# Performance work log

Measured on AMD Instinct MI355X. Metric: run time of the kernel, lower is better.

Reference implementation:

```python
import jax, jax.numpy as jnp
import numpy as np

N = 100000   # nodes
E = 400000   # edges
G = 5000     # graphs (20 nodes each)
H = 128      # hidden_channels
ATOM_D, BOND_D, BOOL_D = 16, 8, 2
NODE_D = 30 + ATOM_D + 3 * BOOL_D   # 52
EDGE_D = 2 + BOND_D + 3 * BOOL_D    # 16


def setup_inputs() -> dict:
    key = jax.random.key(0)
    ks = jax.random.split(key, 24)
    rn = lambda k, shape: jax.random.normal(k, shape, dtype=jnp.float32) * 0.05
    # node features: [atom_idx, 10 continuous, 3 bools]
    atom_idx = jax.random.randint(ks[0], (N,), 1, 119)
    node_cont = jax.random.normal(ks[1], (N, 10), dtype=jnp.float32)
    node_bool = jax.random.randint(ks[2], (N, 3), 0, 2)
    x = jnp.concatenate([atom_idx[:, None].astype(jnp.float32), node_cont,
                         node_bool.astype(jnp.float32)], axis=1)
    # edge features: [bond_idx, 1 continuous, 3 bools]
    bond_idx = jax.random.randint(ks[3], (E,), 1, 22)
    edge_cont = jax.random.normal(ks[4], (E, 1), dtype=jnp.float32)
    edge_bool = jax.random.randint(ks[5], (E, 3), 0, 2)
    edge_attr = jnp.concatenate([bond_idx[:, None].astype(jnp.float32), edge_cont,
                                 edge_bool.astype(jnp.float32)], axis=1)
    edge_index = jax.random.randint(ks[6], (2, E), 0, N)
    batch = jnp.repeat(jnp.arange(G, dtype=jnp.int32), N // G)
    # embeddings (with padding rows zeroed, as nn.Embedding padding_idx)
    atom_emb = rn(ks[7], (119, ATOM_D)).at[0].set(0.0)
    bond_emb = rn(ks[8], (22, BOND_D)).at[0].set(0.0)
    bool_emb = rn(ks[9], (3, BOOL_D)).at[2].set(0.0)
    Wn = rn(ks[10], (10, 30)); bn = jnp.zeros((30,), jnp.float32)
    We = rn(ks[11], (1, 2));   be = jnp.zeros((2,), jnp.float32)
    Wl1 = rn(ks[12], (NODE_D, H)); bl1 = jnp.zeros((H,), jnp.float32)
    Wr1 = rn(ks[13], (NODE_D, H)); br1 = jnp.zeros((H,), jnp.float32)
    Wedge1 = rn(ks[14], (EDGE_D, H)); att1 = rn(ks[15], (H,))
    bias1 = jnp.zeros((H,), jnp.float32)
    Wl2 = rn(ks[16], (H, H)); bl2 = jnp.zeros((H,), jnp.float32)
    Wr2 = rn(ks[17], (H, H)); br2 = jnp.zeros((H,), jnp.float32)
    Wedge2 = rn(ks[18], (EDGE_D, H)); att2 = rn(ks[19], (H,))
    bias2 = jnp.zeros((H,), jnp.float32)
    return dict(x=x, edge_index=edge_index, edge_attr=edge_attr, batch=batch,
                atom_emb=atom_emb, bond_emb=bond_emb, bool_emb=bool_emb,
                Wn=Wn, bn=bn, We=We, be=be,
                Wl1=Wl1, bl1=bl1, Wr1=Wr1, br1=br1, Wedge1=Wedge1, att1=att1, bias1=bias1,
                Wl2=Wl2, bl2=bl2, Wr2=Wr2, br2=br2, Wedge2=Wedge2, att2=att2, bias2=bias2)


def _gatv2(h, src, dst, e_lin, Wl, bl, Wr, br, att, bias):
    # PyG GATv2Conv, heads=1: xl = lin_l(x) (source), xr = lin_r(x) (target)
    xl = h @ Wl + bl
    xr = h @ Wr + br
    m = xl[src] + xr[dst] + e_lin                      # [E', H]
    a = jax.nn.leaky_relu(m, 0.2) @ att                # [E']
    amax = jax.ops.segment_max(a, dst, num_segments=N)
    ex = jnp.exp(a - amax[dst])
    denom = jax.ops.segment_sum(ex, dst, num_segments=N)
    alpha = ex / denom[dst]                            # softmax over incoming edges
    out = jax.ops.segment_sum(alpha[:, None] * xl[src], dst, num_segments=N)
    return out + bias


def reference(x, edge_index, edge_attr, batch,
              atom_emb, bond_emb, bool_emb, Wn, bn, We, be,
              Wl1, bl1, Wr1, br1, Wedge1, att1, bias1,
              Wl2, bl2, Wr2, br2, Wedge2, att2, bias2):
    # --- encode nodes ---
    ai = x[:, 0].astype(jnp.int32)
    nb = x[:, 11:14].astype(jnp.int32)
    h = jnp.concatenate([atom_emb[ai], x[:, 1:11] @ Wn + bn,
                         bool_emb[nb[:, 0]], bool_emb[nb[:, 1]], bool_emb[nb[:, 2]]], axis=1)
    # --- encode edges ---
    bi = edge_attr[:, 0].astype(jnp.int32)
    eb = edge_attr[:, 2:5].astype(jnp.int32)
    e = jnp.concatenate([bond_emb[bi], edge_attr[:, 1:2] @ We + be,
                         bool_emb[eb[:, 0]], bool_emb[eb[:, 1]], bool_emb[eb[:, 2]]], axis=1)
    src, dst = edge_index[0], edge_index[1]
    # --- add self loops with fill_value='mean' (mean of in-edge attrs per node) ---
    cnt = jax.ops.segment_sum(jnp.ones((E,), h.dtype), dst, num_segments=N)
    loop_attr = jax.ops.segment_sum(e, dst, num_segments=N) / jnp.maximum(cnt, 1.0)[:, None]
    e_full = jnp.concatenate([e, loop_attr], axis=0)          # [E+N, EDGE_D]
    loop = jnp.arange(N, dtype=src.dtype)
    src_f = jnp.concatenate([src, loop])
    dst_f = jnp.concatenate([dst, loop])
    # --- 3 GATv2 layers (layers 2 and 3 share weights, as in the original) ---
    h = jax.nn.relu(_gatv2(h, src_f, dst_f, e_full @ Wedge1, Wl1, bl1, Wr1, br1, att1, bias1))
    e_lin2 = e_full @ Wedge2
    h = jax.nn.relu(_gatv2(h, src_f, dst_f, e_lin2, Wl2, bl2, Wr2, br2, att2, bias2))
    h = jax.nn.relu(_gatv2(h, src_f, dst_f, e_lin2, Wl2, bl2, Wr2, br2, att2, bias2))
    # --- global_max_pool readout ---
    return jax.ops.segment_max(h, batch, num_segments=G)
```

## Files before the change

### kernel.cpp

```cpp
#include <hip/hip_runtime.h>
#include <hip/hip_fp16.h>

#define N_NODES 100000
#define N_EDGES 400000
#define N_GRAPHS 5000
#define NPG 20
#define SCAN_NB 256
#define SCAN_CHUNK ((N_NODES + SCAN_NB - 1) / SCAN_NB)
#define TAB_STRIDE (256 * 128 + 128)
#define F1 8192
#define F2 16384
#define NB_ENC ((N_NODES + 255) / 256)
#define NB_HIST ((N_EDGES + 255) / 256)

typedef __attribute__((ext_vector_type(8))) _Float16 f16x8;
typedef __attribute__((ext_vector_type(2))) _Float16 h2;
typedef __attribute__((ext_vector_type(4))) float f32x4;

#define DPP_QUAD_XOR1 0xB1
#define DPP_QUAD_XOR2 0x4E
#define DPP_ROW_HALF_MIRROR 0x141
#define DPP_ROW_MIRROR 0x140
template <int CTRL>
__device__ __forceinline__ float dpp_add(float x) {
  int p = __builtin_amdgcn_update_dpp(0, __float_as_int(x), CTRL, 0xf, 0xf, true);
  return x + __int_as_float(p);
}

__global__ __launch_bounds__(256) void k_prologue(
    const float* __restrict__ x, const float* __restrict__ atom_emb,
    const float* __restrict__ bool_emb, const float* __restrict__ Wn,
    const float* __restrict__ bn, __half* __restrict__ h0,
    const int* __restrict__ dst, int* __restrict__ cnt,
    const float* __restrict__ Wedge1, const float* __restrict__ Wedge2,
    const float* __restrict__ bond_emb, const float* __restrict__ We,
    const float* __restrict__ be, __half* __restrict__ tabs,
    const float* __restrict__ Wl1, const float* __restrict__ Wr1,
    const float* __restrict__ Wl2, const float* __restrict__ Wr2,
    unsigned short* __restrict__ fr) {
  int b = blockIdx.x, tid = threadIdx.x;
  if (b < NB_ENC) {
    int n = b * 256 + tid;
    if (n >= N_NODES) return;
    const float* xr = x + (size_t)n * 14;
    int ai = (int)xr[0];
    _Float16 hr[64];
    #pragma unroll
    for (int j = 0; j < 16; j++) hr[j] = (_Float16)atom_emb[ai * 16 + j];
    float xc[10];
    #pragma unroll
    for (int k = 0; k < 10; k++) xc[k] = xr[1 + k];
    #pragma unroll
    for (int c = 0; c < 30; c++) {
      float s = bn[c];
      #pragma unroll
      for (int k = 0; k < 10; k++) s += xc[k] * Wn[k * 30 + c];
      hr[16 + c] = (_Float16)s;
    }
    #pragma unroll
    for (int t = 0; t < 3; t++) {
      int bb = (int)xr[11 + t];
      hr[46 + 2 * t]     = (_Float16)bool_emb[2 * bb];
      hr[46 + 2 * t + 1] = (_Float16)bool_emb[2 * bb + 1];
    }
    #pragma unroll
    for (int j = 52; j < 64; j++) hr[j] = (_Float16)0.0f;
    uint4* d4 = (uint4*)(h0 + (size_t)n * 64);
    const uint4* s4 = (const uint4*)hr;
    #pragma unroll
    for (int j = 0; j < 8; j++) d4[j] = s4[j];
  } else if (b < NB_ENC + NB_HIST) {
    int e = (b - NB_ENC) * 256 + tid;
    if (e >= N_EDGES) return;
    atomicAdd(cnt + dst[e], 1);
  } else if (b == NB_ENC + NB_HIST) {
    int s = tid >> 7, c = tid & 127;
    const float* W = s ? Wedge2 : Wedge1;
    __half* T12 = tabs + (size_t)s * TAB_STRIDE;
    __half* v   = T12 + 256 * 128;
    float w8 = W[8 * 128 + c], w9 = W[9 * 128 + c];
    v[c] = __float2half(We[0] * w8 + We[1] * w9);
    float cst = be[0] * w8 + be[1] * w9;
    float bond[22];
    for (int bb = 0; bb < 22; bb++) {
      float acc = 0.f;
      #pragma unroll
      for (int k = 0; k < 8; k++) acc += bond_emb[bb * 8 + k] * W[k * 128 + c];
      bond[bb] = acc;
    }
    for (int combo = 0; combo < 8; combo++) {
      float t2 = cst;
      #pragma unroll
      for (int tt = 0; tt < 3; tt++) {
        int bt = (combo >> tt) & 1;
        t2 += bool_emb[bt * 2 + 0] * W[(10 + 2 * tt + 0) * 128 + c];
        t2 += bool_emb[bt * 2 + 1] * W[(10 + 2 * tt + 1) * 128 + c];
      }
      for (int bb = 0; bb < 22; bb++)
        T12[(combo * 32 + bb) * 128 + c] = __float2half(bond[bb] + t2);
      for (int bb = 22; bb < 32; bb++)
        T12[(combo * 32 + bb) * 128 + c] = __float2half(0.f);
    }
  } else {
    int g = (b - (NB_ENC + NB_HIST + 1)) * 256 + tid;
    const float* W; int K; unsigned short* base; int fl;
    if (g < 1024)      { W = Wl1; K = 52;  base = fr;               fl = g; }
    else if (g < 2048) { W = Wr1; K = 52;  base = fr + F1;          fl = g - 1024; }
    else if (g < 4096) { W = Wl2; K = 128; base = fr + 2 * F1;      fl = g - 2048; }
    else if (g < 6144) { W = Wr2; K = 128; base = fr + 2 * F1 + F2; fl = g - 4096; }
    else return;
    int l = fl & 63, ctn = fl >> 6;
    int tn = ctn & 7, c = ctn >> 3;
    int n = tn * 16 + (l & 15);
    int kb = c * 32 + (l >> 4) * 8;
    unsigned h8[8];
    #pragma unroll
    for (int j = 0; j < 8; j++) {
      int k = kb + j;
      float v = (k < K) ? W[(size_t)k * 128 + n] : 0.f;
      __half hv = __float2half(v);
      h8[j] = (unsigned)*(unsigned short*)&hv;
    }
    uint4 hv4 = make_uint4(h8[0] | (h8[1] << 16), h8[2] | (h8[3] << 16),
                           h8[4] | (h8[5] << 16), h8[6] | (h8[7] << 16));
    *(uint4*)(base + (size_t)fl * 8) = hv4;
  }
}

__global__ __launch_bounds__(256) void k_scan1(const int* __restrict__ cnt,
                                               int* __restrict__ bsum) {
  __shared__ int red[256];
  int b = blockIdx.x, t = threadIdx.x;
  int beg = b * SCAN_CHUNK;
  int end = beg + SCAN_CHUNK; if (end > N_NODES) end = N_NODES;
  int s = 0;
  for (int i = beg + t; i < end; i += 256) s += cnt[i] + 1;
  red[t] = s;
  __syncthreads();
  for (int off = 128; off > 0; off >>= 1) {
    if (t < off) red[t] += red[t + off];
    __syncthreads();
  }
  if (t == 0) bsum[b] = red[0];
}

__global__ __launch_bounds__(256) void k_scan3(const int* __restrict__ cnt,
                                               const int* __restrict__ bsum,
                                               int* __restrict__ indptr,
                                               int* __restrict__ cursor) {
  __shared__ int sh[256];
  __shared__ int carry;
  int b = blockIdx.x, t = threadIdx.x;
  sh[t] = bsum[t];
  __syncthreads();
  for (int off = 1; off < 256; off <<= 1) {
    int v = (t >= off) ? sh[t - off] : 0;
    __syncthreads();
    sh[t] += v;
    __syncthreads();
  }
  if (t == 0) carry = (b > 0) ? sh[b - 1] : 0;
  __syncthreads();
  int beg = b * SCAN_CHUNK;
  int end = beg + SCAN_CHUNK; if (end > N_NODES) end = N_NODES;
  for (int base = beg; base < end; base += 256) {
    int i = base + t;
    int v = (i < end) ? cnt[i] + 1 : 0;
    sh[t] = v;
    __syncthreads();
    for (int off = 1; off < 256; off <<= 1) {
      int u = (t >= off) ? sh[t - off] : 0;
      __syncthreads();
      sh[t] += u;
      __syncthreads();
    }
    int excl = sh[t] - v;
    if (i < end) {
      int val = carry + excl;
      indptr[i] = val;
      cursor[i] = val;
    }
    __syncthreads();
    if (t == 255) carry += sh[255];
    __syncthreads();
  }
  if (b == 0 && t == 0) indptr[N_NODES] = N_EDGES + N_NODES;
}

__global__ void k_fill(const int* __restrict__ srcA,
                       const int* __restrict__ dst,
                       const float* __restrict__ eattr,
                       int* __restrict__ cursor,
                       int4* __restrict__ scode) {
  int e = blockIdx.x * blockDim.x + threadIdx.x;
  if (e >= N_EDGES) return;
  const float* r = eattr + (size_t)e * 5;
  int bi = (int)r[0];
  float ec = r[1];
  int combo = (int)r[2] + 2 * (int)r[3] + 4 * (int)r[4];
  int meta = bi | (combo << 5);
  int d = dst[e];
  int p = atomicAdd(&cursor[d], 1);
  scode[p] = make_int4(srcA[e], meta, __float_as_int(ec), 0);
}

template <int KPAD>
__global__ __launch_bounds__(256, 4) void k_gemm2m(const __half* __restrict__ A,
                                                   const unsigned short* __restrict__ WfL,
                                                   const unsigned short* __restrict__ WfR,
                                                   const float* __restrict__ bl_,
                                                   const float* __restrict__ br_,
                                                   __half* __restrict__ outl,
                                                   __half* __restrict__ outr) {
  __shared__ unsigned short Bs[2][8192];
  const int tid = threadIdx.x;
  const int wv = tid >> 6, lane = tid & 63;
  const int tw = blockIdx.x * 4 + wv;
  const bool active = (tw < N_NODES / 16);
  const int ml = lane & 15, q = lane >> 4;
  const int m0 = active ? tw * 16 : 0;
  f32x4 accL[8], accR[8];
  #pragma unroll
  for (int t = 0; t < 8; t++) {
    accL[t] = (f32x4){0.f, 0.f, 0.f, 0.f};
    accR[t] = (f32x4){0.f, 0.f, 0.f, 0.f};
  }
  const _Float16* ar0 = (const _Float16*)A + (size_t)(m0 + ml) * KPAD + q * 8;
  constexpr int NC2 = KPAD / 64;
  for (int c2 = 0; c2 < NC2; c2++) {
    #pragma unroll
    for (int i0 = 0; i0 < 1024; i0 += 256) {
      int i = i0 + tid;
      size_t g = ((size_t)c2 * 1024 + i) * 8;
      *(uint4*)(&Bs[0][i * 8]) = *(const uint4*)(WfL + g);
      *(uint4*)(&Bs[1][i * 8]) = *(const uint4*)(WfR + g);
    }
    __syncthreads();
    #pragma unroll
    for (int sub = 0; sub < 2; sub++) {
      f16x8 a = *(const f16x8*)(ar0 + c2 * 64 + sub * 32);
      #pragma unroll
      for (int t = 0; t < 8; t++) {
        int idx = (sub * 512 + t * 64 + lane) * 8;
        f16x8 bL = *(const f16x8*)(&Bs[0][idx]);
        f16x8 bR = *(const f16x8*)(&Bs[1][idx]);
        accL[t] = __builtin_amdgcn_mfma_f32_16x16x32_f16(a, bL, accL[t], 0, 0, 0);
        accR[t] = __builtin_amdgcn_mfma_f32_16x16x32_f16(a, bR, accR[t], 0, 0, 0);
      }
    }
    __syncthreads();
  }
  __syncthreads();
  if (!active) return;
  __half* eb = (__half*)&Bs[0][0] + wv * 2048;
  const int srow = q * 4;
  const int rrow0 = lane >> 4;
  const int rcol = (lane & 15) * 8;
  #pragma unroll
  for (int t = 0; t < 8; t++) {
    int n = t * 16 + ml;
    float bL = bl_[n];
    #pragma unroll
    for (int r = 0; r < 4; r++)
      eb[(srow + r) * 128 + n] = __float2half(accL[t][r] + bL);
  }
  #pragma unroll
  for (int pp = 0; pp < 4; pp++) {
    uint4 v = *(const uint4*)(eb + pp * 512 + lane * 8);
    *(uint4*)(outl + (size_t)(m0 + pp * 4 + rrow0) * 128 + rcol) = v;
  }
  #pragma unroll
  for (int t = 0; t < 8; t++) {
    int n = t * 16 + ml;
    float bR = br_[n];
    #pragma unroll
    for (int r = 0; r < 4; r++)
      eb[(srow + r) * 128 + n] = __float2half(accR[t][r] + bR);
  }
  #pragma unroll
  for (int pp = 0; pp < 4; pp++) {
    uint4 v = *(const uint4*)(eb + pp * 512 + lane * 8);
    *(uint4*)(outr + (size_t)(m0 + pp * 4 + rrow0) * 128 + rcol) = v;
  }
}

__global__ __launch_bounds__(256) void k_gat(const __half* __restrict__ xl,
                                             const __half* __restrict__ xr,
                                             const int* __restrict__ indptr,
                                             const int4* __restrict__ scode,
                                             const __half* __restrict__ tabs,
                                             const float* __restrict__ att,
                                             const float* __restrict__ bias,
                                             __half* __restrict__ hout) {
  int wid = (blockIdx.x * 256 + threadIdx.x) >> 6;
  int nw = (gridDim.x * 256) >> 6;
  int lane = threadIdx.x & 63;
  int q4 = lane >> 4;
  int c = (lane & 15) * 8;
  const __half* T12 = tabs;
  uint4 vu = *(const uint4*)(tabs + 256 * 128 + c);
  h2 v4[4] = {*reinterpret_cast<h2*>(&vu.x), *reinterpret_cast<h2*>(&vu.y),
              *reinterpret_cast<h2*>(&vu.z), *reinterpret_cast<h2*>(&vu.w)};
  float4 af0 = *(const float4*)(att + c);
  float4 af1 = *(const float4*)(att + c + 4);
  h2 a4[4] = {{(_Float16)af0.x, (_Float16)af0.y}, {(_Float16)af0.z, (_Float16)af0.w},
              {(_Float16)af1.x, (_Float16)af1.y}, {(_Float16)af1.z, (_Float16)af1.w}};
  float bb[8];
  {
    float4 b0 = *(const float4*)(bias + c);
    float4 b1 = *(const float4*)(bias + c + 4);
    bb[0] = b0.x; bb[1] = b0.y; bb[2] = b0.z; bb[3] = b0.w;
    bb[4] = b1.x; bb[5] = b1.y; bb[6] = b1.z; bb[7] = b1.w;
  }
  const h2 z2 = {(_Float16)0.f, (_Float16)0.f};
  const h2 k2 = {(_Float16)0.2f, (_Float16)0.2f};
  wid = __builtin_amdgcn_readfirstlane(wid);
  const int stride = nw * 4;
  int nb = wid * 4;
  if (nb >= N_NODES) return;
  int n = nb + q4;
  int bg = indptr[n], en = indptr[n + 1];
  uint4 xru = *(const uint4*)(xr + (size_t)n * 128 + c);
  while (true) {
    int nb2 = nb + stride;
    bool has2 = (nb2 < N_NODES);
    int n2 = has2 ? nb2 + q4 : n;
    int bg2 = indptr[n2];
    int en2 = indptr[n2 + 1];
    uint4 xru2 = *(const uint4*)(xr + (size_t)n2 * 128 + c);
    int beg = bg, end1 = en - 1;
    int last = (end1 > beg) ? end1 - 1 : beg;
    h2 xrv[4] = {*reinterpret_cast<h2*>(&xru.x), *reinterpret_cast<h2*>(&xru.y),
                 *reinterpret_cast<h2*>(&xru.z), *reinterpret_cast<h2*>(&xru.w)};
    float denom = 0.f;
    float acc[8] = {0.f, 0.f, 0.f, 0.f, 0.f, 0.f, 0.f, 0.f};
    h2 els[4] = {z2, z2, z2, z2};
    int my_it = (end1 - beg + 3) >> 2;
    int m1 = my_it, m2;
    m2 = __shfl_xor(m1, 16, 64); m1 = m1 > m2 ? m1 : m2;
    m2 = __shfl_xor(m1, 32, 64); m1 = m1 > m2 ? m1 : m2;
    int iters = m1;
    for (int it = 0; it < iters; it++) {
      int j = beg + it * 4;
      int4 sc4[4]; h2 xlv[4][4]; float tt[4];
      bool val[4];
      #pragma unroll
      for (int u = 0; u < 4; u++) {
        val[u] = (j + u < end1);
        int jj = val[u] ? j + u : last;
        sc4[u] = scode[jj];
      }
      #pragma unroll
      for (int u = 0; u < 4; u++) {
        int s = val[u] ? sc4[u].x : n;
        uint4 lv = *(const uint4*)(xl + (size_t)s * 128 + c);
        xlv[u][0] = *reinterpret_cast<h2*>(&lv.x);
        xlv[u][1] = *reinterpret_cast<h2*>(&lv.y);
        xlv[u][2] = *reinterpret_cast<h2*>(&lv.z);
        xlv[u][3] = *reinterpret_cast<h2*>(&lv.w);
      }
      #pragma unroll
      for (int u = 0; u < 4; u++) {
        int meta = val[u] ? (sc4[u].y & 255) : 255;
        float ec = val[u] ? __int_as_float(sc4[u].z) : 0.f;
        uint4 tv = *(const uint4*)(T12 + (size_t)meta * 128 + c);
        h2 t4[4] = {*reinterpret_cast<h2*>(&tv.x), *reinterpret_cast<h2*>(&tv.y),
                    *reinterpret_cast<h2*>(&tv.z), *reinterpret_cast<h2*>(&tv.w)};
        _Float16 eh = (_Float16)ec;
        h2 eh2 = {eh, eh};
        h2 d = z2;
        #pragma unroll
        for (int k = 0; k < 4; k++) {
          h2 el = eh2 * v4[k] + t4[k];
          h2 m = xlv[u][k] + xrv[k] + el;
          h2 l = __builtin_elementwise_max(m, z2) + k2 * __builtin_elementwise_min(m, z2);
          d += l * a4[k];
          els[k] += el;
        }
        tt[u] = (float)d[0] + (float)d[1];
      }
      #pragma unroll
      for (int u = 0; u < 4; u++) tt[u] = dpp_add<DPP_QUAD_XOR1>(tt[u]);
      #pragma unroll
      for (int u = 0; u < 4; u++) tt[u] = dpp_add<DPP_QUAD_XOR2>(tt[u]);
      #pragma unroll
      for (int u = 0; u < 4; u++) tt[u] = dpp_add<DPP_ROW_HALF_MIRROR>(tt[u]);
      #pragma unroll
      for (int u = 0; u < 4; u++) tt[u] = dpp_add<DPP_ROW_MIRROR>(tt[u]);
      #pragma unroll
      for (int u = 0; u < 4; u++) {
        float ex = val[u] ? __expf(tt[u]) : 0.f;
        denom += ex;
        #pragma unroll
        for (int k = 0; k < 4; k++) {
          acc[2 * k]     += ex * (float)xlv[u][k][0];
          acc[2 * k + 1] += ex * (float)xlv[u][k][1];
        }
      }
    }
    int cntn = end1 - beg;
    float inv_cnt = 1.0f / (float)(cntn > 0 ? cntn : 1);
    uint4 xnu = *(const uint4*)(xl + (size_t)n * 128 + c);
    h2 xn[4] = {*reinterpret_cast<h2*>(&xnu.x), *reinterpret_cast<h2*>(&xnu.y),
                *reinterpret_cast<h2*>(&xnu.z), *reinterpret_cast<h2*>(&xnu.w)};
    float afv[8] = {af0.x, af0.y, af0.z, af0.w, af1.x, af1.y, af1.z, af1.w};
    float ts = 0.f;
    float xnf[8];
    #pragma unroll
    for (int k = 0; k < 4; k++) {
      #pragma unroll
      for (int hh = 0; hh < 2; hh++) {
        int i = 2 * k + hh;
        xnf[i] = (float)xn[k][hh];
        float m = xnf[i] + (float)xrv[k][hh] + (float)els[k][hh] * inv_cnt;
        float l = m > 0.f ? m : 0.2f * m;
        ts += l * afv[i];
      }
    }
    ts = dpp_add<DPP_QUAD_XOR1>(ts);
    ts = dpp_add<DPP_QUAD_XOR2>(ts);
    ts = dpp_add<DPP_ROW_HALF_MIRROR>(ts);
    ts = dpp_add<DPP_ROW_MIRROR>(ts);
    float ex = __expf(ts);
    denom += ex;
    #pragma unroll
    for (int i = 0; i < 8; i++) acc[i] += ex * xnf[i];
    float invd = 1.0f / denom;
    h2 p[4];
    #pragma unroll
    for (int k = 0; k < 4; k++) {
      float o0 = acc[2 * k] * invd + bb[2 * k];
      float o1 = acc[2 * k + 1] * invd + bb[2 * k + 1];
      o0 = o0 > 0.f ? o0 : 0.f;
      o1 = o1 > 0.f ? o1 : 0.f;
      p[k] = (h2){(_Float16)o0, (_Float16)o1};
    }
    uint4 st = make_uint4(*reinterpret_cast<unsigned*>(&p[0]),
                          *reinterpret_cast<unsigned*>(&p[1]),
                          *reinterpret_cast<unsigned*>(&p[2]),
                          *reinterpret_cast<unsigned*>(&p[3]));
    *(uint4*)(hout + (size_t)n * 128 + c) = st;
    if (!has2) break;
    nb = nb2; n = n2; bg = bg2; en = en2; xru = xru2;
  }
}

__global__ void k_readout(const __half* __restrict__ h, float* __restrict__ out) {
  int wid = (blockIdx.x * blockDim.x + threadIdx.x) >> 6;
  int lane = threadIdx.x & 63;
  if (wid >= N_GRAPHS) return;
  int c = lane * 2;
  float m0 = -1e30f, m1 = -1e30f;
  for (int i = 0; i < NPG; i++) {
    unsigned v = *(const unsigned*)(h + ((size_t)(wid * NPG + i)) * 128 + c);
    h2 f = *reinterpret_cast<h2*>(&v);
    m0 = fmaxf(m0, (float)f[0]);
    m1 = fmaxf(m1, (float)f[1]);
  }
  float2 o; o.x = m0; o.y = m1;
  *(float2*)(out + (size_t)wid * 128 + c) = o;
}

extern "C" void kernel_launch(void* const* d_in, const int* in_sizes, int n_in,
                              void* d_out, int out_size, void* d_ws, size_t ws_size,
                              hipStream_t stream) {
  (void)in_sizes; (void)n_in; (void)out_size; (void)ws_size;
  const float* x        = (const float*)d_in[0];
  const int*   eindex   = (const int*)d_in[1];
  const float* eattr    = (const float*)d_in[2];
  const float* atom_emb = (const float*)d_in[4];
  const float* bond_emb = (const float*)d_in[5];
  const float* bool_emb = (const float*)d_in[6];
  const float* Wn   = (const float*)d_in[7];
  const float* bn   = (const float*)d_in[8];
  const float* We   = (const float*)d_in[9];
  const float* be   = (const float*)d_in[10];
  const float* Wl1  = (const float*)d_in[11];
  const float* bl1  = (const float*)d_in[12];
  const float* Wr1  = (const float*)d_in[13];
  const float* br1  = (const float*)d_in[14];
  const float* Wedge1 = (const float*)d_in[15];
  const float* att1 = (const float*)d_in[16];
  const float* bias1 = (const float*)d_in[17];
  const float* Wl2  = (const float*)d_in[18];
  const float* bl2  = (const float*)d_in[19];
  const float* Wr2  = (const float*)d_in[20];
  const float* br2  = (const float*)d_in[21];
  const float* Wedge2 = (const float*)d_in[22];
  const float* att2 = (const float*)d_in[23];
  const float* bias2 = (const float*)d_in[24];

  const int* srcA = eindex;
  const int* dstA = eindex + N_EDGES;

  char* p = (char*)d_ws;
  auto alloc = [&](size_t bytes) {
    char* r = p;
    p += (bytes + 255) & ~(size_t)255;
    return r;
  };
  __half* h0     = (__half*)alloc((size_t)N_NODES * 64 * 2);
  __half* h      = (__half*)alloc((size_t)N_NODES * 128 * 2);
  __half* xl     = (__half*)alloc((size_t)N_NODES * 128 * 2);
  __half* xrb    = (__half*)alloc((size_t)N_NODES * 128 * 2);
  int*    cnt    = (int*)alloc((size_t)N_NODES * 4);
  int*    indptr = (int*)alloc((size_t)(N_NODES + 1) * 4);
  int*    cursor = (int*)alloc((size_t)N_NODES * 4);
  int4*   scode  = (int4*)alloc((size_t)(N_EDGES + N_NODES) * 16);
  __half* tabs   = (__half*)alloc((size_t)2 * TAB_STRIDE * 2);
  unsigned short* wfrag = (unsigned short*)alloc((size_t)(2 * F1 + 2 * F2) * 2);
  int*    bsum   = (int*)alloc((size_t)SCAN_NB * 4);

  (void)hipMemsetAsync(cnt, 0, (size_t)N_NODES * 4, stream);

  k_prologue<<<NB_ENC + NB_HIST + 1 + 24, 256, 0, stream>>>(
      x, atom_emb, bool_emb, Wn, bn, h0, dstA, cnt,
      Wedge1, Wedge2, bond_emb, We, be, tabs,
      Wl1, Wr1, Wl2, Wr2, wfrag);
  k_scan1<<<SCAN_NB, 256, 0, stream>>>(cnt, bsum);
  k_scan3<<<SCAN_NB, 256, 0, stream>>>(cnt, bsum, indptr, cursor);
  k_fill<<<(N_EDGES + 255) / 256, 256, 0, stream>>>(srcA, dstA, eattr, cursor, scode);

  const unsigned short* f_l1 = wfrag;
  const unsigned short* f_r1 = wfrag + F1;
  const unsigned short* f_l2 = wfrag + 2 * F1;
  const unsigned short* f_r2 = wfrag + 2 * F1 + F2;

  const int GB2 = (N_NODES / 16 + 3) / 4;

  k_gemm2m<64><<<GB2, 256, 0, stream>>>(h0, f_l1, f_r1, bl1, br1, xl, xrb);
  k_gat<<<2048, 256, 0, stream>>>(xl, xrb, indptr, scode, tabs, att1, bias1, h);

  k_gemm2m<128><<<GB2, 256, 0, stream>>>(h, f_l2, f_r2, bl2, br2, xl, xrb);
  k_gat<<<2048, 256, 0, stream>>>(xl, xrb, indptr, scode, tabs + TAB_STRIDE, att2, bias2, h);

  k_gemm2m<128><<<GB2, 256, 0, stream>>>(h, f_l2, f_r2, bl2, br2, xl, xrb);
  k_gat<<<2048, 256, 0, stream>>>(xl, xrb, indptr, scode, tabs + TAB_STRIDE, att2, bias2, h);

  k_readout<<<(N_GRAPHS * 64 + 255) / 256, 256, 0, stream>>>(h, (float*)d_out);
}
```

Before: 344.4 us.

## Sort nodes by in-degree so GAT wave quads get balanced work

Builds a degree histogram during the scan, prefix-sums it, and in the fill kernel produces a permutation of nodes bucketed by in-degree (capped at 63). The GAT kernel then walks nodes in that permuted order, so the four nodes sharing a wave have similar edge counts and the per-wave max-iteration loop wastes fewer lanes. This costs an extra indirection load per node, extra atomics in scan/fill, and loses the locality of contiguous node ordering for xr/hout accesses.

After: 334.6 us. -2.9%, faster.

```diff
diff --git a/kernel.cpp b/kernel.cpp
--- a/kernel.cpp
+++ b/kernel.cpp
@@ -128,13 +128,21 @@
 }
 
 __global__ __launch_bounds__(256) void k_scan1(const int* __restrict__ cnt,
-                                               int* __restrict__ bsum) {
+                                               int* __restrict__ bsum,
+                                               int* __restrict__ ghist) {
   __shared__ int red[256];
+  __shared__ int lh[64];
   int b = blockIdx.x, t = threadIdx.x;
+  if (t < 64) lh[t] = 0;
+  __syncthreads();
   int beg = b * SCAN_CHUNK;
   int end = beg + SCAN_CHUNK; if (end > N_NODES) end = N_NODES;
   int s = 0;
-  for (int i = beg + t; i < end; i += 256) s += cnt[i] + 1;
+  for (int i = beg + t; i < end; i += 256) {
+    int cv = cnt[i];
+    s += cv + 1;
+    atomicAdd(&lh[cv < 63 ? cv : 63], 1);
+  }
   red[t] = s;
   __syncthreads();
   for (int off = 128; off > 0; off >>= 1) {
@@ -142,12 +150,15 @@
     __syncthreads();
   }
   if (t == 0) bsum[b] = red[0];
+  if (t < 64 && lh[t] > 0) atomicAdd(&ghist[t], lh[t]);
 }
 
 __global__ __launch_bounds__(256) void k_scan3(const int* __restrict__ cnt,
                                                const int* __restrict__ bsum,
                                                int* __restrict__ indptr,
-                                               int* __restrict__ cursor) {
+                                               int* __restrict__ cursor,
+                                               const int* __restrict__ ghist,
+                                               int* __restrict__ gcur) {
   __shared__ int sh[256];
   __shared__ int carry;
   int b = blockIdx.x, t = threadIdx.x;
@@ -185,23 +196,57 @@
     __syncthreads();
   }
   if (b == 0 && t == 0) indptr[N_NODES] = N_EDGES + N_NODES;
+  if (b == 0) {
+    __syncthreads();
+    if (t < 64) sh[t] = ghist[t];
+    __syncthreads();
+    if (t == 0) {
+      int run = 0;
+      for (int i = 0; i < 64; i++) { int v = sh[i]; sh[i] = run; run += v; }
+    }
+    __syncthreads();
+    if (t < 64) gcur[t] = sh[t];
+  }
 }
 
 __global__ void k_fill(const int* __restrict__ srcA,
                        const int* __restrict__ dst,
                        const float* __restrict__ eattr,
                        int* __restrict__ cursor,
-                       int4* __restrict__ scode) {
-  int e = blockIdx.x * blockDim.x + threadIdx.x;
-  if (e >= N_EDGES) return;
-  const float* r = eattr + (size_t)e * 5;
-  int bi = (int)r[0];
-  float ec = r[1];
-  int combo = (int)r[2] + 2 * (int)r[3] + 4 * (int)r[4];
-  int meta = bi | (combo << 5);
-  int d = dst[e];
-  int p = atomicAdd(&cursor[d], 1);
-  scode[p] = make_int4(srcA[e], meta, __float_as_int(ec), 0);
+                       int4* __restrict__ scode,
+                       const int* __restrict__ cnt,
+                       int* __restrict__ gcur,
+                       int* __restrict__ perm) {
+  int b = blockIdx.x, t = threadIdx.x;
+  if (b < NB_HIST) {
+    int e = b * 256 + t;
+    if (e >= N_EDGES) return;
+    const float* r = eattr + (size_t)e * 5;
+    int bi = (int)r[0];
+    float ec = r[1];
+    int combo = (int)r[2] + 2 * (int)r[3] + 4 * (int)r[4];
+    int meta = bi | (combo << 5);
+    int d = dst[e];
+    int p = atomicAdd(&cursor[d], 1);
+    scode[p] = make_int4(srcA[e], meta, __float_as_int(ec), 0);
+  } else {
+    __shared__ int lh[64];
+    __shared__ int lbase[64];
+    if (t < 64) lh[t] = 0;
+    __syncthreads();
+    int n = (b - NB_HIST) * 256 + t;
+    bool v = (n < N_NODES);
+    int dc = 0, r = 0;
+    if (v) {
+      int cv = cnt[n];
+      dc = cv < 63 ? cv : 63;
+      r = atomicAdd(&lh[dc], 1);
+    }
+    __syncthreads();
+    if (t < 64 && lh[t] > 0) lbase[t] = atomicAdd(&gcur[t], lh[t]);
+    __syncthreads();
+    if (v) perm[lbase[dc] + r] = n;
+  }
 }
 
 template <int KPAD>
@@ -291,7 +336,8 @@
                                              const __half* __restrict__ tabs,
                                              const float* __restrict__ att,
                                              const float* __restrict__ bias,
-                                             __half* __restrict__ hout) {
+                                             __half* __restrict__ hout,
+                                             const int* __restrict__ perm) {
   int wid = (blockIdx.x * 256 + threadIdx.x) >> 6;
   int nw = (gridDim.x * 256) >> 6;
   int lane = threadIdx.x & 63;
@@ -318,13 +364,13 @@
   const int stride = nw * 4;
   int nb = wid * 4;
   if (nb >= N_NODES) return;
-  int n = nb + q4;
+  int n = perm[nb + q4];
   int bg = indptr[n], en = indptr[n + 1];
   uint4 xru = *(const uint4*)(xr + (size_t)n * 128 + c);
   while (true) {
     int nb2 = nb + stride;
     bool has2 = (nb2 < N_NODES);
-    int n2 = has2 ? nb2 + q4 : n;
+    int n2 = has2 ? perm[nb2 + q4] : n;
     int bg2 = indptr[n2];
     int en2 = indptr[n2 + 1];
     uint4 xru2 = *(const uint4*)(xr + (size_t)n2 * 128 + c);
@@ -510,16 +556,21 @@
   __half* tabs   = (__half*)alloc((size_t)2 * TAB_STRIDE * 2);
   unsigned short* wfrag = (unsigned short*)alloc((size_t)(2 * F1 + 2 * F2) * 2);
   int*    bsum   = (int*)alloc((size_t)SCAN_NB * 4);
+  int*    ghist  = (int*)alloc((size_t)64 * 4);
+  int*    gcur   = (int*)alloc((size_t)64 * 4);
+  int*    perm   = (int*)alloc((size_t)N_NODES * 4);
 
   (void)hipMemsetAsync(cnt, 0, (size_t)N_NODES * 4, stream);
+  (void)hipMemsetAsync(ghist, 0, (size_t)64 * 4, stream);
 
   k_prologue<<<NB_ENC + NB_HIST + 1 + 24, 256, 0, stream>>>(
       x, atom_emb, bool_emb, Wn, bn, h0, dstA, cnt,
       Wedge1, Wedge2, bond_emb, We, be, tabs,
       Wl1, Wr1, Wl2, Wr2, wfrag);
-  k_scan1<<<SCAN_NB, 256, 0, stream>>>(cnt, bsum);
-  k_scan3<<<SCAN_NB, 256, 0, stream>>>(cnt, bsum, indptr, cursor);
-  k_fill<<<(N_EDGES + 255) / 256, 256, 0, stream>>>(srcA, dstA, eattr, cursor, scode);
+  k_scan1<<<SCAN_NB, 256, 0, stream>>>(cnt, bsum, ghist);
+  k_scan3<<<SCAN_NB, 256, 0, stream>>>(cnt, bsum, indptr, cursor, ghist, gcur);
+  k_fill<<<NB_HIST + NB_ENC, 256, 0, stream>>>(srcA, dstA, eattr, cursor, scode,
+                                               cnt, gcur, perm);
 
   const unsigned short* f_l1 = wfrag;
   const unsigned short* f_r1 = wfrag + F1;
@@ -529,13 +580,13 @@
   const int GB2 = (N_NODES / 16 + 3) / 4;
 
   k_gemm2m<64><<<GB2, 256, 0, stream>>>(h0, f_l1, f_r1, bl1, br1, xl, xrb);
-  k_gat<<<2048, 256, 0, stream>>>(xl, xrb, indptr, scode, tabs, att1, bias1, h);
+  k_gat<<<2048, 256, 0, stream>>>(xl, xrb, indptr, scode, tabs, att1, bias1, h, perm);
 
   k_gemm2m<128><<<GB2, 256, 0, stream>>>(h, f_l2, f_r2, bl2, br2, xl, xrb);
-  k_gat<<<2048, 256, 0, stream>>>(xl, xrb, indptr, scode, tabs + TAB_STRIDE, att2, bias2, h);
+  k_gat<<<2048, 256, 0, stream>>>(xl, xrb, indptr, scode, tabs + TAB_STRIDE, att2, bias2, h, perm);
 
   k_gemm2m<128><<<GB2, 256, 0, stream>>>(h, f_l2, f_r2, bl2, br2, xl, xrb);
-  k_gat<<<2048, 256, 0, stream>>>(xl, xrb, indptr, scode, tabs + TAB_STRIDE, att2, bias2, h);
+  k_gat<<<2048, 256, 0, stream>>>(xl, xrb, indptr, scode, tabs + TAB_STRIDE, att2, bias2, h, perm);
 
   k_readout<<<(N_GRAPHS * 64 + 255) / 256, 256, 0, stream>>>(h, (float*)d_out);
 }
```
